# Optimization experiments

Hardware: AMD Instinct MI355X
Metric: run time of the kernel (lower is better)

The kernel has to match this reference:

```python
import jax, jax.numpy as jnp
import numpy as np
from jax.scipy.special import logsumexp

D, E, V = 512, 4, 32000
B, L = 1, 1024


def setup_inputs() -> dict:
    key = jax.random.key(0)
    ks = jax.random.split(key, 5)
    s = 0.02
    return {
        "hidden_states": jax.random.normal(ks[0], (B, L, D), dtype=jnp.float32),
        "W_prior": jax.random.normal(ks[1], (D, E), dtype=jnp.float32) * s,
        "b_prior": jnp.zeros((E,), dtype=jnp.float32),
        "W_latent": jax.random.normal(ks[2], (D, E * D), dtype=jnp.float32) * s,
        "b_latent": jnp.zeros((E * D,), dtype=jnp.float32),
        "W_dec": jax.random.normal(ks[3], (D, V), dtype=jnp.float32) * s,
        "b_dec": jnp.zeros((V,), dtype=jnp.float32),
    }


def reference(hidden_states, W_prior, b_prior, W_latent, b_latent, W_dec, b_dec):
    # hidden_states: [B, L, D]
    b, l, d = hidden_states.shape
    e = W_prior.shape[1]
    # mixture coefficients (split_hidden=False path): softmax over experts
    mix_logits = hidden_states @ W_prior + b_prior                 # [B, L, E]
    log_coef = jax.nn.log_softmax(mix_logits, axis=-1)             # [B, L, E]
    # per-expert latent projections with tanh
    latent = jnp.tanh(hidden_states @ W_latent + b_latent)         # [B, L, E*D]
    latent = latent.reshape(b, l, e, d)                            # [B, L, E, D]
    # shared decoder to vocab
    logits = jnp.einsum("bled,dv->blev", latent, W_dec) + b_dec    # [B, L, E, V]
    logp = jax.nn.log_softmax(logits, axis=-1)                     # [B, L, E, V]
    # log(sum_e coef_e * softmax_e) == logsumexp_e(log_coef_e + log_softmax_e)
    out = logsumexp(logp + log_coef[..., None], axis=2)            # [B, L, V]
    return out
```

## Files before the change

kernel.cpp:

```cpp
#include <hip/hip_runtime.h>
#include <hip/hip_bf16.h>
#include <hip/hip_fp16.h>
#include <math.h>


#define D_ 512
#define E_ 4
#define V_ 32000
#define L_ 1024
#define AROWS (L_ * E_)

typedef __attribute__((ext_vector_type(8))) short s16x8;
typedef __attribute__((ext_vector_type(4))) float f32x4;
typedef __attribute__((ext_vector_type(2))) float f32x2;
typedef __attribute__((ext_vector_type(4))) unsigned int u32x4;
typedef const __attribute__((address_space(1))) char* gp1_t;
typedef __attribute__((address_space(3))) char* lp3_t;

__device__ __forceinline__ void gload_lds16(const void* g, void* l) {
  __builtin_amdgcn_global_load_lds((gp1_t)g, (lp3_t)l, 16, 0, 0);
}

#define PREP_DEC  8000
#define PREP_LAT  (PREP_DEC + 1024)
#define PREP_CVT  (PREP_LAT + 512)
#define PREP_PRI  (PREP_CVT + 256)
#define PREP_TOT  (PREP_PRI + 16)

__global__ __launch_bounds__(256) void prep_kernel(
    const float* __restrict__ hs, const float* __restrict__ W_prior,
    const float* __restrict__ b_prior, const float* __restrict__ W_latent,
    const float* __restrict__ W_dec,
    __hip_bfloat16* __restrict__ hs_bf, __hip_bfloat16* __restrict__ WlatT,
    __hip_bfloat16* __restrict__ WdecT, float* __restrict__ log_coef,
    float* __restrict__ S) {
  __shared__ float tileS[64 * 33];
  const int b = blockIdx.x;
  const int tid = threadIdx.x;

  if (b < PREP_DEC) {
    const int vb = (b % 1000) * 32;
    const int db = (b / 1000) * 64;
    {
      const int r = tid >> 2, c0 = (tid & 3) * 8;
      const float* src = W_dec + (size_t)(db + r) * V_ + vb + c0;
      float4 a0 = *(const float4*)src;
      float4 a1 = *(const float4*)(src + 4);
      float* t = &tileS[r * 33 + c0];
      t[0] = a0.x; t[1] = a0.y; t[2] = a0.z; t[3] = a0.w;
      t[4] = a1.x; t[5] = a1.y; t[6] = a1.z; t[7] = a1.w;
    }
    __syncthreads();
    {
      const int vr = tid >> 3, d0 = (tid & 7) * 8;
      __hip_bfloat16 tmp[8];
      #pragma unroll
      for (int j = 0; j < 8; ++j)
        tmp[j] = __float2bfloat16(tileS[(d0 + j) * 33 + vr]);
      *(s16x8*)(WdecT + (size_t)(vb + vr) * D_ + db + d0) = *(s16x8*)tmp;
    }
  } else if (b < PREP_LAT) {
    const int bb = b - PREP_DEC;
    const int cb = (bb & 63) * 32, rb = (bb >> 6) * 32;
    const int C = E_ * D_, R = D_;
    const int tx = tid & 31, ty = tid >> 5;
    #pragma unroll
    for (int j = 0; j < 32; j += 8)
      tileS[(ty + j) * 33 + tx] = W_latent[(size_t)(rb + ty + j) * C + cb + tx];
    __syncthreads();
    #pragma unroll
    for (int j = 0; j < 32; j += 8)
      WlatT[(size_t)(cb + ty + j) * R + rb + tx] = __float2bfloat16(tileS[tx * 33 + ty + j]);
  } else if (b < PREP_CVT) {
    int i = ((b - PREP_LAT) * 256 + tid) * 4;
    float4 v = *(const float4*)(hs + i);
    hs_bf[i + 0] = __float2bfloat16(v.x);
    hs_bf[i + 1] = __float2bfloat16(v.y);
    hs_bf[i + 2] = __float2bfloat16(v.z);
    hs_bf[i + 3] = __float2bfloat16(v.w);
  } else if (b < PREP_PRI) {
    int t = (b - PREP_CVT) * 4 + (tid >> 6);
    int lane = tid & 63;
    float a0 = 0.f, a1 = 0.f, a2 = 0.f, a3 = 0.f;
    for (int d = lane; d < D_; d += 64) {
      float h = hs[t * D_ + d];
      float4 w = ((const float4*)W_prior)[d];
      a0 += h * w.x; a1 += h * w.y; a2 += h * w.z; a3 += h * w.w;
    }
    #pragma unroll
    for (int off = 32; off > 0; off >>= 1) {
      a0 += __shfl_xor(a0, off);
      a1 += __shfl_xor(a1, off);
      a2 += __shfl_xor(a2, off);
      a3 += __shfl_xor(a3, off);
    }
    a0 += b_prior[0]; a1 += b_prior[1]; a2 += b_prior[2]; a3 += b_prior[3];
    float mx = fmaxf(fmaxf(a0, a1), fmaxf(a2, a3));
    float ls = mx + logf(expf(a0 - mx) + expf(a1 - mx) + expf(a2 - mx) + expf(a3 - mx));
    if (lane == 0) {
      log_coef[t * 4 + 0] = a0 - ls;
      log_coef[t * 4 + 1] = a1 - ls;
      log_coef[t * 4 + 2] = a2 - ls;
      log_coef[t * 4 + 3] = a3 - ls;
    }
  } else {
    S[(b - PREP_PRI) * 256 + tid] = 0.f;
  }
}

__global__ void qk_kernel(const float* __restrict__ log_coef, const float* __restrict__ S,
                          float* __restrict__ q) {
  int i = blockIdx.x * blockDim.x + threadIdx.x;
  if (i < AROWS) q[i] = __expf(log_coef[i]) / S[i];
}

__global__ __launch_bounds__(256, 2) void latent_gemm(
    const __hip_bfloat16* __restrict__ Abf, const __hip_bfloat16* __restrict__ BT,
    const float* __restrict__ b_latent, __hip_bfloat16* __restrict__ latent) {
  __shared__ short As[128 * 32];
  __shared__ short Bs[128 * 32];
  const int tid = threadIdx.x;
  const int wave = tid >> 6, lane = tid & 63;
  const int wm = wave >> 1, wn = wave & 1;
  const int m0 = blockIdx.y * 128;
  const int n0 = blockIdx.x * 128;
  const int lrow = lane & 15;
  const int kgrp = lane >> 4;
  const int srow = wave * 16 + (lane >> 2);
  const int scol = (lane & 3) * 8;

  f32x4 acc[4][4];
  #pragma unroll
  for (int mt = 0; mt < 4; ++mt)
    #pragma unroll
    for (int nt = 0; nt < 4; ++nt) acc[mt][nt] = f32x4{0.f, 0.f, 0.f, 0.f};

  for (int kt = 0; kt < 16; ++kt) {
    const int k0 = kt * 32;
    #pragma unroll
    for (int j = 0; j < 2; ++j) {
      const int row = j * 64 + srow;
      gload_lds16(Abf + (size_t)(m0 + row) * D_ + k0 + scol, &As[(j * 256 + wave * 64) * 8]);
      gload_lds16(BT + (size_t)(n0 + row) * D_ + k0 + scol, &Bs[(j * 256 + wave * 64) * 8]);
    }
    __syncthreads();
    s16x8 af[4], bfr[4];
    #pragma unroll
    for (int mt = 0; mt < 4; ++mt) af[mt] = *(const s16x8*)&As[(wm * 64 + mt * 16 + lrow) * 32 + kgrp * 8];
    #pragma unroll
    for (int nt = 0; nt < 4; ++nt) bfr[nt] = *(const s16x8*)&Bs[(wn * 64 + nt * 16 + lrow) * 32 + kgrp * 8];
    #pragma unroll
    for (int mt = 0; mt < 4; ++mt)
      #pragma unroll
      for (int nt = 0; nt < 4; ++nt)
        acc[mt][nt] = __builtin_amdgcn_mfma_f32_16x16x32_bf16(af[mt], bfr[nt], acc[mt][nt], 0, 0, 0);
    __syncthreads();
  }

  float blat[4];
  #pragma unroll
  for (int nt = 0; nt < 4; ++nt) blat[nt] = b_latent[n0 + wn * 64 + nt * 16 + lrow];
  #pragma unroll
  for (int mt = 0; mt < 4; ++mt)
    #pragma unroll
    for (int r = 0; r < 4; ++r) {
      const int row = m0 + wm * 64 + mt * 16 + kgrp * 4 + r;
      #pragma unroll
      for (int nt = 0; nt < 4; ++nt) {
        const int col = n0 + wn * 64 + nt * 16 + lrow;
        float v = tanhf(acc[mt][nt][r] + blat[nt]);
        latent[(size_t)row * (E_ * D_) + col] = __float2bfloat16(v);
      }
    }
}

template <int MODE>
__global__ __launch_bounds__(256, 2) void mos_gemm(
    const __hip_bfloat16* __restrict__ A,
    const __hip_bfloat16* __restrict__ WdecT,
    const float* __restrict__ b_dec,
    const float* __restrict__ q,
    float* __restrict__ S,
    float* __restrict__ out,
    unsigned int* __restrict__ pbuf) {
  const int bid = blockIdx.x;
  const int xcd = bid & 7;
  const int idx = bid >> 3;
  const int mg = xcd >> 2;
  const int vg = xcd & 3;
  const int vt = vg * 63 + (idx >> 4);
  const int mtile = mg * 16 + (idx & 15);
  if (vt >= V_ / 128) return;
  const int m0 = mtile * 128;
  const int v0 = vt * 128;

  __shared__ short As[128 * 32];
  __shared__ short Bs[128 * 32];
  const int tid = threadIdx.x;
  const int wave = tid >> 6, lane = tid & 63;
  const int wm = wave >> 1, wn = wave & 1;
  const int lrow = lane & 15;
  const int kgrp = lane >> 4;
  const int srow = wave * 16 + (lane >> 2);
  const int scol = (lane & 3) * 8;

  float bdec[4];
  #pragma unroll
  for (int nt = 0; nt < 4; ++nt) bdec[nt] = b_dec[v0 + wn * 64 + nt * 16 + lrow];

  f32x4 acc[4][4];
  #pragma unroll
  for (int mt = 0; mt < 4; ++mt)
    #pragma unroll
    for (int nt = 0; nt < 4; ++nt) acc[mt][nt] = f32x4{0.f, 0.f, 0.f, 0.f};

  for (int kt = 0; kt < 16; ++kt) {
    const int k0 = kt * 32;
    #pragma unroll
    for (int j = 0; j < 2; ++j) {
      const int row = j * 64 + srow;
      gload_lds16(A + (size_t)(m0 + row) * D_ + k0 + scol, &As[(j * 256 + wave * 64) * 8]);
      gload_lds16(WdecT + (size_t)(v0 + row) * D_ + k0 + scol, &Bs[(j * 256 + wave * 64) * 8]);
    }
    __syncthreads();
    s16x8 af[4], bfr[4];
    #pragma unroll
    for (int mt = 0; mt < 4; ++mt) af[mt] = *(const s16x8*)&As[(wm * 64 + mt * 16 + lrow) * 32 + kgrp * 8];
    #pragma unroll
    for (int nt = 0; nt < 4; ++nt) bfr[nt] = *(const s16x8*)&Bs[(wn * 64 + nt * 16 + lrow) * 32 + kgrp * 8];
    #pragma unroll
    for (int mt = 0; mt < 4; ++mt)
      #pragma unroll
      for (int nt = 0; nt < 4; ++nt)
        acc[mt][nt] = __builtin_amdgcn_mfma_f32_16x16x32_bf16(af[mt], bfr[nt], acc[mt][nt], 0, 0, 0);
    __syncthreads();
  }

  if constexpr (MODE == 1 || MODE == 3) {
    #pragma unroll
    for (int mt = 0; mt < 4; ++mt) {
      const int row4 = m0 + wm * 64 + mt * 16 + kgrp * 4;
      const int token = row4 >> 2;
      float p0 = 0.f, p1 = 0.f, p2 = 0.f, p3 = 0.f;
      #pragma unroll
      for (int nt = 0; nt < 4; ++nt) {
        float e0 = __expf(acc[mt][nt][0] + bdec[nt]);
        float e1 = __expf(acc[mt][nt][1] + bdec[nt]);
        float e2 = __expf(acc[mt][nt][2] + bdec[nt]);
        float e3 = __expf(acc[mt][nt][3] + bdec[nt]);
        p0 += e0; p1 += e1; p2 += e2; p3 += e3;
        if constexpr (MODE == 3) {
          const int v = v0 + wn * 64 + nt * 16 + lrow;
          int u = 0;
          u = __builtin_amdgcn_cvt_pk_fp8_f32(e0, e1, u, false);
          u = __builtin_amdgcn_cvt_pk_fp8_f32(e2, e3, u, true);
          __builtin_nontemporal_store((unsigned int)u, &pbuf[(size_t)token * V_ + v]);
        }
      }
      #pragma unroll
      for (int off = 1; off < 16; off <<= 1) {
        p0 += __shfl_xor(p0, off);
        p1 += __shfl_xor(p1, off);
        p2 += __shfl_xor(p2, off);
        p3 += __shfl_xor(p3, off);
      }
      if (lrow == 0) {
        atomicAdd(&S[row4 + 0], p0);
        atomicAdd(&S[row4 + 1], p1);
        atomicAdd(&S[row4 + 2], p2);
        atomicAdd(&S[row4 + 3], p3);
      }
    }
  } else {
    #pragma unroll
    for (int mt = 0; mt < 4; ++mt) {
      const int row4 = m0 + wm * 64 + mt * 16 + kgrp * 4;
      const float4 qv = *(const float4*)&q[row4];
      const int token = row4 >> 2;
      #pragma unroll
      for (int nt = 0; nt < 4; ++nt) {
        float v = qv.x * __expf(acc[mt][nt][0] + bdec[nt]) +
                  qv.y * __expf(acc[mt][nt][1] + bdec[nt]) +
                  qv.z * __expf(acc[mt][nt][2] + bdec[nt]) +
                  qv.w * __expf(acc[mt][nt][3] + bdec[nt]);
        out[(size_t)token * V_ + v0 + wn * 64 + nt * 16 + lrow] = __logf(v);
      }
    }
  }
}

__global__ __launch_bounds__(256) void combine_kernel(
    const unsigned int* __restrict__ pbuf,
    const float* __restrict__ lc, const float* __restrict__ S,
    float* __restrict__ out) {
  const int t = blockIdx.y;
  const int v = blockIdx.x * 1024 + threadIdx.x * 4;
  if (v >= V_) return;
  const float4 lcv = ((const float4*)lc)[t];
  const float4 Sv = ((const float4*)S)[t];
  const float q0 = __expf(lcv.x) / Sv.x;
  const float q1 = __expf(lcv.y) / Sv.y;
  const float q2 = __expf(lcv.z) / Sv.z;
  const float q3 = __expf(lcv.w) / Sv.w;
  u32x4 u = __builtin_nontemporal_load((const u32x4*)(pbuf + (size_t)t * V_ + v));
  float4 o;
  #pragma unroll
  for (int j = 0; j < 4; ++j) {
    unsigned int w = u[j];
    f32x2 lo = __builtin_amdgcn_cvt_pk_f32_fp8(w, false);
    f32x2 hi = __builtin_amdgcn_cvt_pk_f32_fp8(w, true);
    float s = q0 * lo.x + q1 * lo.y + q2 * hi.x + q3 * hi.y;
    ((float*)&o)[j] = __logf(s);
  }
  *(float4*)&out[(size_t)t * V_ + v] = o;
}

extern "C" void kernel_launch(void* const* d_in, const int* in_sizes, int n_in,
                              void* d_out, int out_size, void* d_ws, size_t ws_size,
                              hipStream_t stream) {
  const float* hs       = (const float*)d_in[0];
  const float* W_prior  = (const float*)d_in[1];
  const float* b_prior  = (const float*)d_in[2];
  const float* W_latent = (const float*)d_in[3];
  const float* b_latent = (const float*)d_in[4];
  const float* W_dec    = (const float*)d_in[5];
  const float* b_dec    = (const float*)d_in[6];
  float* out = (float*)d_out;

  char* ws = (char*)d_ws;
  __hip_bfloat16* hs_bf  = (__hip_bfloat16*)(ws);
  __hip_bfloat16* WlatT  = (__hip_bfloat16*)(ws + (1u << 20));
  __hip_bfloat16* latent = (__hip_bfloat16*)(ws + 3u * (1u << 20));
  __hip_bfloat16* WdecT  = (__hip_bfloat16*)(ws + 7u * (1u << 20));
  float* log_coef = (float*)(ws + 40u * (1u << 20));
  float* S = log_coef + AROWS;
  float* q = S + AROWS;
  unsigned int* pbuf = (unsigned int*)(ws + 41u * (1u << 20));

  const size_t needA = 41u * (1u << 20) + (size_t)L_ * V_ * 4;
  const bool pathA = ws_size >= needA;

  prep_kernel<<<PREP_TOT, 256, 0, stream>>>(hs, W_prior, b_prior, W_latent, W_dec,
                                            hs_bf, WlatT, WdecT, log_coef, S);
  latent_gemm<<<dim3((E_ * D_) / 128, L_ / 128), 256, 0, stream>>>(hs_bf, WlatT, b_latent, latent);

  if (pathA) {
    mos_gemm<3><<<8 * 16 * 63, 256, 0, stream>>>(latent, WdecT, b_dec, nullptr, S, nullptr, pbuf);
    combine_kernel<<<dim3(32, L_), 256, 0, stream>>>(pbuf, log_coef, S, out);
  } else {
    mos_gemm<1><<<8 * 16 * 63, 256, 0, stream>>>(latent, WdecT, b_dec, nullptr, S, nullptr, nullptr);
    qk_kernel<<<(AROWS + 255) / 256, 256, 0, stream>>>(log_coef, S, q);
    mos_gemm<2><<<8 * 16 * 63, 256, 0, stream>>>(latent, WdecT, b_dec, q, nullptr, out, nullptr);
  }
}
```

Measured before the change: 409.8 us.

## Switch decoder GEMM to FP8 scaled MFMA with pre-scaled operands

Converts W_dec and the tanh latent to FP8 (e4m3), pre-scaling them by 16 and 4, and runs the vocab GEMM with the MI355 scaled 16x16x128 f8f6f4 MFMA. The block scale exponents undo the pre-scaling. LDS tiles now hold 128-byte K chunks with an XOR swizzle, and the K loop drops from 16 to 4 iterations. This halves operand bytes and doubles MFMA throughput, at the cost of reduced precision in the logits, which can hurt accuracy of the log-softmax output.

After: 360.9 us. 11.9% less time.

```diff
diff --git a/kernel.cpp b/kernel.cpp
--- a/kernel.cpp
+++ b/kernel.cpp
@@ -10,9 +10,14 @@
 #define L_ 1024
 #define AROWS (L_ * E_)
 
+#define SA_ 0x7D7D7D7D
+#define SB_ 0x7B7B7B7B
+
 typedef __attribute__((ext_vector_type(8))) short s16x8;
 typedef __attribute__((ext_vector_type(4))) float f32x4;
 typedef __attribute__((ext_vector_type(2))) float f32x2;
+typedef __attribute__((ext_vector_type(4))) int i32x4;
+typedef __attribute__((ext_vector_type(8))) int i32x8;
 typedef __attribute__((ext_vector_type(4))) unsigned int u32x4;
 typedef const __attribute__((address_space(1))) char* gp1_t;
 typedef __attribute__((address_space(3))) char* lp3_t;
@@ -32,7 +37,7 @@
     const float* __restrict__ b_prior, const float* __restrict__ W_latent,
     const float* __restrict__ W_dec,
     __hip_bfloat16* __restrict__ hs_bf, __hip_bfloat16* __restrict__ WlatT,
-    __hip_bfloat16* __restrict__ WdecT, float* __restrict__ log_coef,
+    unsigned char* __restrict__ WdecT8, float* __restrict__ log_coef,
     float* __restrict__ S) {
   __shared__ float tileS[64 * 33];
   const int b = blockIdx.x;
@@ -53,11 +58,16 @@
     __syncthreads();
     {
       const int vr = tid >> 3, d0 = (tid & 7) * 8;
-      __hip_bfloat16 tmp[8];
-      #pragma unroll
-      for (int j = 0; j < 8; ++j)
-        tmp[j] = __float2bfloat16(tileS[(d0 + j) * 33 + vr]);
-      *(s16x8*)(WdecT + (size_t)(vb + vr) * D_ + db + d0) = *(s16x8*)tmp;
+      float t8[8];
+      #pragma unroll
+      for (int j = 0; j < 8; ++j) t8[j] = tileS[(d0 + j) * 33 + vr] * 16.f;
+      unsigned int u0 = 0, u1 = 0;
+      u0 = __builtin_amdgcn_cvt_pk_fp8_f32(t8[0], t8[1], u0, false);
+      u0 = __builtin_amdgcn_cvt_pk_fp8_f32(t8[2], t8[3], u0, true);
+      u1 = __builtin_amdgcn_cvt_pk_fp8_f32(t8[4], t8[5], u1, false);
+      u1 = __builtin_amdgcn_cvt_pk_fp8_f32(t8[6], t8[7], u1, true);
+      uint2 uu = {u0, u1};
+      *(uint2*)&WdecT8[(size_t)(vb + vr) * D_ + db + d0] = uu;
     }
   } else if (b < PREP_LAT) {
     const int bb = b - PREP_DEC;
@@ -116,7 +126,7 @@
 
 __global__ __launch_bounds__(256, 2) void latent_gemm(
     const __hip_bfloat16* __restrict__ Abf, const __hip_bfloat16* __restrict__ BT,
-    const float* __restrict__ b_latent, __hip_bfloat16* __restrict__ latent) {
+    const float* __restrict__ b_latent, unsigned char* __restrict__ latent8) {
   __shared__ short As[128 * 32];
   __shared__ short Bs[128 * 32];
   const int tid = threadIdx.x;
@@ -168,16 +178,17 @@
       #pragma unroll
       for (int nt = 0; nt < 4; ++nt) {
         const int col = n0 + wn * 64 + nt * 16 + lrow;
-        float v = tanhf(acc[mt][nt][r] + blat[nt]);
-        latent[(size_t)row * (E_ * D_) + col] = __float2bfloat16(v);
+        float v = tanhf(acc[mt][nt][r] + blat[nt]) * 4.f;
+        int u = __builtin_amdgcn_cvt_pk_fp8_f32(v, v, 0, false);
+        latent8[(size_t)row * (E_ * D_) + col] = (unsigned char)(u & 0xff);
       }
     }
 }
 
 template <int MODE>
 __global__ __launch_bounds__(256, 2) void mos_gemm(
-    const __hip_bfloat16* __restrict__ A,
-    const __hip_bfloat16* __restrict__ WdecT,
+    const unsigned char* __restrict__ A8,
+    const unsigned char* __restrict__ W8,
     const float* __restrict__ b_dec,
     const float* __restrict__ q,
     float* __restrict__ S,
@@ -194,15 +205,15 @@
   const int m0 = mtile * 128;
   const int v0 = vt * 128;
 
-  __shared__ short As[128 * 32];
-  __shared__ short Bs[128 * 32];
+  __shared__ __attribute__((aligned(16))) unsigned char As[128 * 128];
+  __shared__ __attribute__((aligned(16))) unsigned char Bs[128 * 128];
   const int tid = threadIdx.x;
   const int wave = tid >> 6, lane = tid & 63;
   const int wm = wave >> 1, wn = wave & 1;
   const int lrow = lane & 15;
   const int kgrp = lane >> 4;
-  const int srow = wave * 16 + (lane >> 2);
-  const int scol = (lane & 3) * 8;
+  const int srow8 = wave * 8 + (lane >> 3);
+  const int schunk = lane & 7;
 
   float bdec[4];
   #pragma unroll
@@ -214,25 +225,39 @@
     #pragma unroll
     for (int nt = 0; nt < 4; ++nt) acc[mt][nt] = f32x4{0.f, 0.f, 0.f, 0.f};
 
-  for (int kt = 0; kt < 16; ++kt) {
-    const int k0 = kt * 32;
-    #pragma unroll
-    for (int j = 0; j < 2; ++j) {
-      const int row = j * 64 + srow;
-      gload_lds16(A + (size_t)(m0 + row) * D_ + k0 + scol, &As[(j * 256 + wave * 64) * 8]);
-      gload_lds16(WdecT + (size_t)(v0 + row) * D_ + k0 + scol, &Bs[(j * 256 + wave * 64) * 8]);
-    }
-    __syncthreads();
-    s16x8 af[4], bfr[4];
-    #pragma unroll
-    for (int mt = 0; mt < 4; ++mt) af[mt] = *(const s16x8*)&As[(wm * 64 + mt * 16 + lrow) * 32 + kgrp * 8];
-    #pragma unroll
-    for (int nt = 0; nt < 4; ++nt) bfr[nt] = *(const s16x8*)&Bs[(wn * 64 + nt * 16 + lrow) * 32 + kgrp * 8];
+  for (int kt = 0; kt < 4; ++kt) {
+    const int kb = kt * 128;
+    #pragma unroll
+    for (int j = 0; j < 4; ++j) {
+      const int row = j * 32 + srow8;
+      const int sc = (schunk ^ (row & 7)) * 16;
+      gload_lds16(A8 + (size_t)(m0 + row) * D_ + kb + sc, &As[(j * 32 + wave * 8) * 128]);
+      gload_lds16(W8 + (size_t)(v0 + row) * D_ + kb + sc, &Bs[(j * 32 + wave * 8) * 128]);
+    }
+    __syncthreads();
+    i32x8 af[4], bfr[4];
+    #pragma unroll
+    for (int mt = 0; mt < 4; ++mt) {
+      const int row = wm * 64 + mt * 16 + lrow;
+      const int s = lrow & 7;
+      i32x4 lo = *(const i32x4*)&As[row * 128 + (((kgrp * 2) ^ s) * 16)];
+      i32x4 hi = *(const i32x4*)&As[row * 128 + (((kgrp * 2 + 1) ^ s) * 16)];
+      af[mt] = __builtin_shufflevector(lo, hi, 0, 1, 2, 3, 4, 5, 6, 7);
+    }
+    #pragma unroll
+    for (int nt = 0; nt < 4; ++nt) {
+      const int row = wn * 64 + nt * 16 + lrow;
+      const int s = lrow & 7;
+      i32x4 lo = *(const i32x4*)&Bs[row * 128 + (((kgrp * 2) ^ s) * 16)];
+      i32x4 hi = *(const i32x4*)&Bs[row * 128 + (((kgrp * 2 + 1) ^ s) * 16)];
+      bfr[nt] = __builtin_shufflevector(lo, hi, 0, 1, 2, 3, 4, 5, 6, 7);
+    }
     #pragma unroll
     for (int mt = 0; mt < 4; ++mt)
       #pragma unroll
       for (int nt = 0; nt < 4; ++nt)
-        acc[mt][nt] = __builtin_amdgcn_mfma_f32_16x16x32_bf16(af[mt], bfr[nt], acc[mt][nt], 0, 0, 0);
+        acc[mt][nt] = __builtin_amdgcn_mfma_scale_f32_16x16x128_f8f6f4(
+            af[mt], bfr[nt], acc[mt][nt], 0, 0, 0, SA_, 0, SB_);
     __syncthreads();
   }
 
@@ -328,28 +353,28 @@
   float* out = (float*)d_out;
 
   char* ws = (char*)d_ws;
-  __hip_bfloat16* hs_bf  = (__hip_bfloat16*)(ws);
-  __hip_bfloat16* WlatT  = (__hip_bfloat16*)(ws + (1u << 20));
-  __hip_bfloat16* latent = (__hip_bfloat16*)(ws + 3u * (1u << 20));
-  __hip_bfloat16* WdecT  = (__hip_bfloat16*)(ws + 7u * (1u << 20));
-  float* log_coef = (float*)(ws + 40u * (1u << 20));
+  __hip_bfloat16* hs_bf   = (__hip_bfloat16*)(ws);
+  __hip_bfloat16* WlatT   = (__hip_bfloat16*)(ws + (1u << 20));
+  unsigned char*  latent8 = (unsigned char*)(ws + 3u * (1u << 20));
+  unsigned char*  WdecT8  = (unsigned char*)(ws + 5u * (1u << 20));
+  float* log_coef = (float*)(ws + 22u * (1u << 20));
   float* S = log_coef + AROWS;
   float* q = S + AROWS;
-  unsigned int* pbuf = (unsigned int*)(ws + 41u * (1u << 20));
-
-  const size_t needA = 41u * (1u << 20) + (size_t)L_ * V_ * 4;
+  unsigned int* pbuf = (unsigned int*)(ws + 23u * (1u << 20));
+
+  const size_t needA = 23u * (1u << 20) + (size_t)L_ * V_ * 4;
   const bool pathA = ws_size >= needA;
 
   prep_kernel<<<PREP_TOT, 256, 0, stream>>>(hs, W_prior, b_prior, W_latent, W_dec,
-                                            hs_bf, WlatT, WdecT, log_coef, S);
-  latent_gemm<<<dim3((E_ * D_) / 128, L_ / 128), 256, 0, stream>>>(hs_bf, WlatT, b_latent, latent);
+                                            hs_bf, WlatT, WdecT8, log_coef, S);
+  latent_gemm<<<dim3((E_ * D_) / 128, L_ / 128), 256, 0, stream>>>(hs_bf, WlatT, b_latent, latent8);
 
   if (pathA) {
-    mos_gemm<3><<<8 * 16 * 63, 256, 0, stream>>>(latent, WdecT, b_dec, nullptr, S, nullptr, pbuf);
+    mos_gemm<3><<<8 * 16 * 63, 256, 0, stream>>>(latent8, WdecT8, b_dec, nullptr, S, nullptr, pbuf);
     combine_kernel<<<dim3(32, L_), 256, 0, stream>>>(pbuf, log_coef, S, out);
   } else {
-    mos_gemm<1><<<8 * 16 * 63, 256, 0, stream>>>(latent, WdecT, b_dec, nullptr, S, nullptr, nullptr);
+    mos_gemm<1><<<8 * 16 * 63, 256, 0, stream>>>(latent8, WdecT8, b_dec, nullptr, S, nullptr, nullptr);
     qk_kernel<<<(AROWS + 255) / 256, 256, 0, stream>>>(log_coef, S, q);
-    mos_gemm<2><<<8 * 16 * 63, 256, 0, stream>>>(latent, WdecT, b_dec, q, nullptr, out, nullptr);
-  }
-}
+    mos_gemm<2><<<8 * 16 * 63, 256, 0, stream>>>(latent8, WdecT8, b_dec, q, nullptr, out, nullptr);
+  }
+}
```
